# Optimization experiments

Measured on AMD Instinct MI355X. Metric: run time of the kernel, lower is better.

## Reference

```python
import jax, jax.numpy as jnp
import numpy as np

B = 4
S = 1024          # per-sequence length (equal for all sequences)
HQ = 32           # query heads
HK = 8            # kv heads (GQA)
D = 128           # head dim


def setup_inputs() -> dict:
    key = jax.random.key(0)
    k1, k2, k3 = jax.random.split(key, 3)
    total = B * S
    q = jax.random.normal(k1, (total, HQ, D), dtype=jnp.float32)
    k = jax.random.normal(k2, (total, HK, D), dtype=jnp.float32)
    v = jax.random.normal(k3, (total, HK, D), dtype=jnp.float32)
    cu = (jnp.arange(B + 1, dtype=jnp.int32) * S)
    return {
        "q": q, "k": k, "v": v,
        "cu_seqlens_q": cu, "cu_seqlens_k": cu,
        "max_seqlen_q": S, "max_seqlen_k": S,
    }


def reference(q, k, v, cu_seqlens_q, cu_seqlens_k, max_seqlen_q, max_seqlen_k):
    # Varlen causal GQA attention (prefill path of Attention.forward).
    # All sequences have equal length S = max_seqlen_q, so the packed varlen
    # layout is exactly a reshape to (B, S, H, D) -- same math as the
    # per-sequence Python loop in attention_varlen_func.
    total, Hq, Dh = q.shape
    Hk = k.shape[1]
    g = Hq // Hk                      # GQA group size
    Sq = int(max_seqlen_q)
    Bn = total // Sq
    scale = 1.0 / (Dh ** 0.5)

    qb = q.reshape(Bn, Sq, Hk, g, Dh)  # (B,S,Hk,g,D)
    kb = k.reshape(Bn, Sq, Hk, Dh)     # (B,S,Hk,D)
    vb = v.reshape(Bn, Sq, Hk, Dh)

    scores = jnp.einsum('bqhgd,bkhd->bhgqk', qb, kb) * scale  # (B,Hk,g,S,S)
    causal_mask = jnp.triu(jnp.ones((Sq, Sq), dtype=bool), k=1)
    scores = jnp.where(causal_mask, -jnp.inf, scores)
    attn = jax.nn.softmax(scores, axis=-1)
    out = jnp.einsum('bhgqk,bkhd->bqhgd', attn, vb)           # (B,S,Hk,g,D)
    return out.reshape(total, Hq, Dh)
```

## Files before the change

### kernel.cpp

```cpp
#include <hip/hip_runtime.h>
#include <hip/hip_bf16.h>
#include <stdint.h>


typedef __bf16 v8bf __attribute__((ext_vector_type(8)));
typedef __bf16 v4bf __attribute__((ext_vector_type(4)));
typedef float  v16f __attribute__((ext_vector_type(16)));

#define NB  4
#define NS  1024
#define NHQ 32
#define NHK 8
#define ND  128
#define BQ  128
#define BK  64

#define KOFF(r) (16*((r)>>3) + ((((r)>>2)&1)*4) + ((r)&3))

__device__ __forceinline__ float fexp2(float x) {
  float r; asm("v_exp_f32 %0, %1" : "=v"(r) : "v"(x)); return r;
}
__device__ __forceinline__ float flog2(float x) {
  float r; asm("v_log_f32 %0, %1" : "=v"(r) : "v"(x)); return r;
}

__global__ __launch_bounds__(256)
void prep(const float* __restrict__ kg, const float* __restrict__ vg,
          char* __restrict__ ws)
{
  const int tid = threadIdx.x;
  const int blk = blockIdx.x;
  if (blk < 4096) {
    int gid = blk * 256 + tid;
    int i  = gid & 31;
    int s  = (gid >> 5) & (NS - 1);
    int hk = (gid >> 15) & 7;
    int b  = gid >> 18;
    float4 f = *(const float4*)(kg + ((size_t)((b * NS + s) * NHK + hk)) * ND + 4 * i);
    v4bf kb;
    kb[0]=(__bf16)f.x; kb[1]=(__bf16)f.y; kb[2]=(__bf16)f.z; kb[3]=(__bf16)f.w;
    int t  = s >> 6;
    int c  = (s >> 5) & 1;
    int kk = s & 31;
    int mu = (kk & 3) + 4 * ((kk >> 3) & 1)
           + 8 * (2 * ((kk >> 4) & 1) + ((kk >> 2) & 1));
    int fidx  = c * 8 + (i >> 2);
    int halfb = (i >> 1) & 1;
    int byte  = fidx * 1024 + halfb * 512 + mu * 16 + ((4 * i) & 7) * 2;
    size_t tb = (size_t)((b * 8 + hk) * 16 + t) << 15;
    *(v4bf*)(ws + tb + byte) = kb;
  } else {
    int vid = (blk - 4096) * 256 + tid;
    int d  = vid & 127;
    int g  = (vid >> 7) & 7;
    int t  = (vid >> 10) & 15;
    int hk = (vid >> 14) & 7;
    int b  = vid >> 17;
    const float* vp = vg + ((size_t)((b * NS + t * 64 + g * 8) * NHK + hk)) * ND + d;
    v8bf w;
    #pragma unroll
    for (int e = 0; e < 8; ++e) w[e] = (__bf16)vp[(size_t)e * (NHK * ND)];
    int byte = (d * 8 + (g ^ ((d >> 1) & 7))) * 16;
    size_t tb = (size_t)((b * 8 + hk) * 16 + t) << 15;
    *(v8bf*)(ws + tb + 16384 + byte) = w;
  }
}

__global__ __launch_bounds__(256, 2)
void fattn(const float* __restrict__ qg, const char* __restrict__ kvg,
           float* __restrict__ og)
{
  __shared__ __align__(16) char  KV[2][32768];
  __shared__ __align__(16) float alq[4 * 32];

  const int tid  = threadIdx.x;
  const int lane = tid & 63;
  const int wave = tid >> 6;
  const int half = lane >> 5;
  const int l31  = lane & 31;

  const int bx = blockIdx.x;
  const int hk = bx & 7;
  const int t6 = bx >> 3;
  const int b  = t6 >> 4;
  const int m6 = t6 & 15;
  const int p  = m6 >> 2;
  const int h  = hk * 4 + (m6 & 3);

  const float scale = 0.12751879523604785f;
  const int kvtile = (b * 8 + hk) * 16;

  auto dma = [&](int t_, char* dst) {
    const char* src = kvg + ((size_t)(kvtile + t_) << 15);
    #pragma unroll
    for (int i = 0; i < 8; ++i) {
      int c = wave * 8 + i;
      __builtin_amdgcn_global_load_lds(
        (const __attribute__((address_space(1))) void*)(src + c * 1024 + lane * 16),
        (__attribute__((address_space(3))) void*)(dst + c * 1024),
        16, 0, 0);
    }
  };

  dma(0, KV[0]);
  int cur = 0;

  for (int ph = 0; ph < 2; ++ph) {
    const int qt = ph ? (7 - p) : p;
    const int wv = ph ? (3 - wave) : wave;
    const int q0 = qt * BQ;
    const int wqb = q0 + wv * 32;
    const int qglob = wqb + l31;
    const int ntiles = 2 * (qt + 1);

    v8bf qf[8];
    {
      const float* qp = qg + ((size_t)((b * NS + qglob) * NHQ + h)) * ND + half * 8;
      #pragma unroll
      for (int dM = 0; dM < 8; ++dM) {
        float4 f0 = *(const float4*)(qp + dM * 16);
        float4 f1 = *(const float4*)(qp + dM * 16 + 4);
        v8bf t;
        t[0]=(__bf16)(f0.x*scale); t[1]=(__bf16)(f0.y*scale);
        t[2]=(__bf16)(f0.z*scale); t[3]=(__bf16)(f0.w*scale);
        t[4]=(__bf16)(f1.x*scale); t[5]=(__bf16)(f1.y*scale);
        t[6]=(__bf16)(f1.z*scale); t[7]=(__bf16)(f1.w*scale);
        qf[dM] = t;
      }
    }

    v16f accO[4];
    #pragma unroll
    for (int dt = 0; dt < 4; ++dt)
      #pragma unroll
      for (int e = 0; e < 16; ++e) accO[dt][e] = 0.f;
    float m_run = 8.0f, l_run = 0.f;

    for (int t = 0; t < ntiles; ++t) {
      const int k0 = t * BK;

      asm volatile("s_waitcnt vmcnt(0)" ::: "memory");
      __syncthreads();

      if (t + 1 < ntiles)      dma(t + 1, KV[cur ^ 1]);
      else if (ph == 0)        dma(0, KV[cur ^ 1]);

      if (k0 <= wqb + 31) {
        const char* ksr = KV[cur];
        const char* vtr = KV[cur] + 16384;
        v16f s0, s1;
        #pragma unroll
        for (int e = 0; e < 16; ++e) { s0[e] = 0.f; s1[e] = 0.f; }
        __builtin_amdgcn_s_setprio(1);
        #pragma unroll
        for (int dM = 0; dM < 8; ++dM) {
          v8bf ka = *(const v8bf*)(ksr + dM * 1024 + lane * 16);
          s0 = __builtin_amdgcn_mfma_f32_32x32x16_bf16(ka, qf[dM], s0, 0, 0, 0);
        }
        #pragma unroll
        for (int dM = 0; dM < 8; ++dM) {
          v8bf ka = *(const v8bf*)(ksr + (dM + 8) * 1024 + lane * 16);
          s1 = __builtin_amdgcn_mfma_f32_32x32x16_bf16(ka, qf[dM], s1, 0, 0, 0);
        }
        __builtin_amdgcn_s_setprio(0);
        if (k0 + BK > wqb) {
          #pragma unroll
          for (int r = 0; r < 16; ++r) {
            int key = k0 + KOFF(r) + half * 8;
            if (key > qglob)      s0[r] = -INFINITY;
            if (key + 32 > qglob) s1[r] = -INFINITY;
          }
        }
        #pragma unroll
        for (int r = 0; r < 16; ++r) s0[r] = fexp2(s0[r] - m_run);
        #pragma unroll
        for (int r = 0; r < 16; ++r) s1[r] = fexp2(s1[r] - m_run);
        __builtin_amdgcn_s_setprio(1);
        #pragma unroll
        for (int C = 0; C < 2; ++C) {
          #pragma unroll
          for (int cp = 0; cp < 2; ++cp) {
            v8bf pf;
            #pragma unroll
            for (int e = 0; e < 8; ++e)
              pf[e] = (__bf16)(C == 0 ? s0[cp * 8 + e] : s1[cp * 8 + e]);
            int g = (C * 2 + cp) * 2 + half;
            #pragma unroll
            for (int dt = 0; dt < 4; ++dt) {
              int d = dt * 32 + l31;
              v8bf vb = *(const v8bf*)(vtr + (d * 8 + (g ^ ((l31 >> 1) & 7))) * 16);
              accO[dt] = __builtin_amdgcn_mfma_f32_32x32x16_bf16(pf, vb, accO[dt], 0, 0, 0);
            }
          }
        }
        __builtin_amdgcn_s_setprio(0);
        float rs = 0.f, pm = 0.f;
        #pragma unroll
        for (int r = 0; r < 16; ++r) {
          rs += s0[r] + s1[r];
          pm = fmaxf(pm, fmaxf(s0[r], s1[r]));
        }
        rs += __shfl_xor(rs, 32);
        pm = fmaxf(pm, __shfl_xor(pm, 32));
        if (__builtin_expect(__any(pm > 256.f), 0)) {
          float al = pm > 256.f ? 1.f / pm : 1.f;
          if (half == 0) alq[wave * 32 + l31] = al;
          float4 alf[4];
          #pragma unroll
          for (int c = 0; c < 4; ++c)
            alf[c] = *(const float4*)(&alq[wave * 32 + 8 * c + 4 * half]);
          #pragma unroll
          for (int dt = 0; dt < 4; ++dt)
            #pragma unroll
            for (int r = 0; r < 16; ++r)
              accO[dt][r] *= ((const float*)&alf[r >> 2])[r & 3];
          l_run = (l_run + rs) * al;
          m_run += (pm > 256.f) ? flog2(pm) : 0.f;
        } else {
          l_run += rs;
        }
      }
      cur ^= 1;
    }

    if (half == 0) alq[wave * 32 + l31] = 1.f / l_run;
    float4 invf[4];
    #pragma unroll
    for (int c = 0; c < 4; ++c)
      invf[c] = *(const float4*)(&alq[wave * 32 + 8 * c + 4 * half]);
    #pragma unroll
    for (int dt = 0; dt < 4; ++dt) {
      #pragma unroll
      for (int r = 0; r < 16; ++r) {
        int qrow = (r & 3) + 8 * (r >> 2) + 4 * half;
        float* op = og + ((size_t)((b * NS + wqb + qrow) * NHQ + h)) * ND;
        op[dt * 32 + l31] = accO[dt][r] * ((const float*)&invf[r >> 2])[r & 3];
      }
    }
  }
}

extern "C" void kernel_launch(void* const* d_in, const int* in_sizes, int n_in,
                              void* d_out, int out_size, void* d_ws, size_t ws_size,
                              hipStream_t stream) {
  const float* q = (const float*)d_in[0];
  const float* k = (const float*)d_in[1];
  const float* v = (const float*)d_in[2];
  float* out = (float*)d_out;
  char* ws = (char*)d_ws;
  prep<<<dim3(4096 + 2048), 256, 0, stream>>>(k, v, ws);
  fattn<<<dim3(NB * NHQ * 4), 256, 0, stream>>>(q, ws, out);
}
```

Before: 192.3 us.

## Split K and V prefetch into staggered DMA stages, add nontemporal loads/stores

The single combined K+V tile prefetch is split into separate K and V DMA stages. Each is issued after its own partial waitcnt and barrier, so the next tile's V load overlaps the QK/softmax work and K overlaps PV. Global loads of q/k/v and output stores are also marked nontemporal to reduce cache pollution. The change adds an extra barrier per tile and relies on vmcnt counting being exactly right.

```diff
diff --git a/kernel.cpp b/kernel.cpp
--- a/kernel.cpp
+++ b/kernel.cpp
@@ -6,6 +6,7 @@
 typedef __bf16 v8bf __attribute__((ext_vector_type(8)));
 typedef __bf16 v4bf __attribute__((ext_vector_type(4)));
 typedef float  v16f __attribute__((ext_vector_type(16)));
+typedef float  v4f  __attribute__((ext_vector_type(4)));
 
 #define NB  4
 #define NS  1024
@@ -36,9 +37,10 @@
     int s  = (gid >> 5) & (NS - 1);
     int hk = (gid >> 15) & 7;
     int b  = gid >> 18;
-    float4 f = *(const float4*)(kg + ((size_t)((b * NS + s) * NHK + hk)) * ND + 4 * i);
+    v4f f = __builtin_nontemporal_load(
+        (const v4f*)(kg + ((size_t)((b * NS + s) * NHK + hk)) * ND + 4 * i));
     v4bf kb;
-    kb[0]=(__bf16)f.x; kb[1]=(__bf16)f.y; kb[2]=(__bf16)f.z; kb[3]=(__bf16)f.w;
+    kb[0]=(__bf16)f[0]; kb[1]=(__bf16)f[1]; kb[2]=(__bf16)f[2]; kb[3]=(__bf16)f[3];
     int t  = s >> 6;
     int c  = (s >> 5) & 1;
     int kk = s & 31;
@@ -59,7 +61,8 @@
     const float* vp = vg + ((size_t)((b * NS + t * 64 + g * 8) * NHK + hk)) * ND + d;
     v8bf w;
     #pragma unroll
-    for (int e = 0; e < 8; ++e) w[e] = (__bf16)vp[(size_t)e * (NHK * ND)];
+    for (int e = 0; e < 8; ++e)
+      w[e] = (__bf16)__builtin_nontemporal_load(vp + (size_t)e * (NHK * ND));
     int byte = (d * 8 + (g ^ ((d >> 1) & 7))) * 16;
     size_t tb = (size_t)((b * 8 + hk) * 16 + t) << 15;
     *(v8bf*)(ws + tb + 16384 + byte) = w;
@@ -90,19 +93,31 @@
   const float scale = 0.12751879523604785f;
   const int kvtile = (b * 8 + hk) * 16;
 
-  auto dma = [&](int t_, char* dst) {
+  auto dmaK = [&](int t_, char* dst) {
     const char* src = kvg + ((size_t)(kvtile + t_) << 15);
     #pragma unroll
-    for (int i = 0; i < 8; ++i) {
-      int c = wave * 8 + i;
+    for (int i = 0; i < 4; ++i) {
+      int c = wave * 4 + i;
       __builtin_amdgcn_global_load_lds(
         (const __attribute__((address_space(1))) void*)(src + c * 1024 + lane * 16),
         (__attribute__((address_space(3))) void*)(dst + c * 1024),
         16, 0, 0);
     }
   };
-
-  dma(0, KV[0]);
+  auto dmaV = [&](int t_, char* dst) {
+    const char* src = kvg + ((size_t)(kvtile + t_) << 15) + 16384;
+    #pragma unroll
+    for (int i = 0; i < 4; ++i) {
+      int c = wave * 4 + i;
+      __builtin_amdgcn_global_load_lds(
+        (const __attribute__((address_space(1))) void*)(src + c * 1024 + lane * 16),
+        (__attribute__((address_space(3))) void*)(dst + 16384 + c * 1024),
+        16, 0, 0);
+    }
+  };
+
+  dmaK(0, KV[0]);
+  dmaV(0, KV[0]);
   int cur = 0;
 
   for (int ph = 0; ph < 2; ++ph) {
@@ -118,13 +133,13 @@
       const float* qp = qg + ((size_t)((b * NS + qglob) * NHQ + h)) * ND + half * 8;
       #pragma unroll
       for (int dM = 0; dM < 8; ++dM) {
-        float4 f0 = *(const float4*)(qp + dM * 16);
-        float4 f1 = *(const float4*)(qp + dM * 16 + 4);
+        v4f f0 = __builtin_nontemporal_load((const v4f*)(qp + dM * 16));
+        v4f f1 = __builtin_nontemporal_load((const v4f*)(qp + dM * 16 + 4));
         v8bf t;
-        t[0]=(__bf16)(f0.x*scale); t[1]=(__bf16)(f0.y*scale);
-        t[2]=(__bf16)(f0.z*scale); t[3]=(__bf16)(f0.w*scale);
-        t[4]=(__bf16)(f1.x*scale); t[5]=(__bf16)(f1.y*scale);
-        t[6]=(__bf16)(f1.z*scale); t[7]=(__bf16)(f1.w*scale);
+        t[0]=(__bf16)(f0[0]*scale); t[1]=(__bf16)(f0[1]*scale);
+        t[2]=(__bf16)(f0[2]*scale); t[3]=(__bf16)(f0[3]*scale);
+        t[4]=(__bf16)(f1[0]*scale); t[5]=(__bf16)(f1[1]*scale);
+        t[6]=(__bf16)(f1[2]*scale); t[7]=(__bf16)(f1[3]*scale);
         qf[dM] = t;
       }
     }
@@ -138,17 +153,18 @@
 
     for (int t = 0; t < ntiles; ++t) {
       const int k0 = t * BK;
-
-      asm volatile("s_waitcnt vmcnt(0)" ::: "memory");
+      const bool has_next = (t + 1 < ntiles) || (ph == 0);
+      const int  tn = (t + 1 < ntiles) ? t + 1 : 0;
+      const bool act = (k0 <= wqb + 31);
+      const char* ksr = KV[cur];
+      const char* vtr = KV[cur] + 16384;
+
+      asm volatile("s_waitcnt vmcnt(4)" ::: "memory");
       __syncthreads();
-
-      if (t + 1 < ntiles)      dma(t + 1, KV[cur ^ 1]);
-      else if (ph == 0)        dma(0, KV[cur ^ 1]);
-
-      if (k0 <= wqb + 31) {
-        const char* ksr = KV[cur];
-        const char* vtr = KV[cur] + 16384;
-        v16f s0, s1;
+      if (has_next) dmaK(tn, KV[cur ^ 1]);
+
+      v16f s0, s1;
+      if (act) {
         #pragma unroll
         for (int e = 0; e < 16; ++e) { s0[e] = 0.f; s1[e] = 0.f; }
         __builtin_amdgcn_s_setprio(1);
@@ -175,6 +191,14 @@
         for (int r = 0; r < 16; ++r) s0[r] = fexp2(s0[r] - m_run);
         #pragma unroll
         for (int r = 0; r < 16; ++r) s1[r] = fexp2(s1[r] - m_run);
+      }
+
+      if (has_next) { asm volatile("s_waitcnt vmcnt(4)" ::: "memory"); }
+      else          { asm volatile("s_waitcnt vmcnt(0)" ::: "memory"); }
+      __syncthreads();
+      if (has_next) dmaV(tn, KV[cur ^ 1]);
+
+      if (act) {
         __builtin_amdgcn_s_setprio(1);
         #pragma unroll
         for (int C = 0; C < 2; ++C) {
@@ -234,7 +258,9 @@
       for (int r = 0; r < 16; ++r) {
         int qrow = (r & 3) + 8 * (r >> 2) + 4 * half;
         float* op = og + ((size_t)((b * NS + wqb + qrow) * NHQ + h)) * ND;
-        op[dt * 32 + l31] = accO[dt][r] * ((const float*)&invf[r >> 2])[r & 3];
+        __builtin_nontemporal_store(
+            accO[dt][r] * ((const float*)&invf[r >> 2])[r & 3],
+            op + dt * 32 + l31);
       }
     }
   }
```

Measured after the change: 197.8 us. 2.8% more time.
